# Performance work log

Measured on AMD Instinct MI355X. Metric: run time of the kernel, lower is better.

The kernel has to match this reference:

```python
import jax, jax.numpy as jnp
import numpy as np

B, T, F = 64, 512, 512      # batch, timesteps, raw feature dim
D_IN = 1024                 # input_layer units
H = 1024                    # hidden_units
D_OUT = 128                 # output_size


def setup_inputs() -> dict:
    key = jax.random.key(0)
    ks = jax.random.split(key, 10)
    def glorot(k, shape):
        lim = np.sqrt(6.0 / (shape[0] + shape[1])).astype(np.float32)
        return jax.random.uniform(k, shape, jnp.float32, -lim, lim)
    return {
        "x": jax.random.normal(ks[0], (B, T, F), jnp.float32),
        # input Dense (tanh)
        "Wi": glorot(ks[1], (F, D_IN)),
        "bi": jnp.zeros((D_IN,), jnp.float32),
        # LSTM layer 0: kernel, recurrent kernel, bias (init ones, gate order i,f,c,o)
        "W0": glorot(ks[2], (D_IN, 4 * H)),
        "U0": glorot(ks[3], (H, 4 * H)),
        "b0": jnp.ones((4 * H,), jnp.float32),
        # LSTM layer 1
        "W1": glorot(ks[4], (H, 4 * H)),
        "U1": glorot(ks[5], (H, 4 * H)),
        "b1": jnp.ones((4 * H,), jnp.float32),
        # output Dense (tanh)
        "Wo": glorot(ks[6], (H, D_OUT)),
        "bo": jnp.zeros((D_OUT,), jnp.float32),
    }


def _lstm_cell(x, h, c, W, U, b):
    # Keras LSTMCell gate order: i, f, c(candidate), o
    z = x @ W + h @ U + b                      # [B, 4H]
    zi, zf, zc, zo = jnp.split(z, 4, axis=-1)
    i = jax.nn.sigmoid(zi)
    f = jax.nn.sigmoid(zf)
    c_new = f * c + i * jnp.tanh(zc)
    h_new = jax.nn.sigmoid(zo) * jnp.tanh(c_new)
    return h_new, c_new


def reference(x, Wi, bi, W0, U0, b0, W1, U1, b1, Wo, bo):
    b = x.shape[0]
    h = W0.shape[1] // 4
    zeros = jnp.zeros((b, h), x.dtype)
    init = (zeros, zeros, zeros, zeros)  # h0, c0, h1, c1

    def step(carry, xt):
        h0, c0, h1, c1 = carry
        xin = jnp.tanh(xt @ Wi + bi)                    # input Dense
        h0, c0 = _lstm_cell(xin, h0, c0, W0, U0, b0)
        h1, c1 = _lstm_cell(h0, h1, c1, W1, U1, b1)
        return (h0, c0, h1, c1), None

    (h0, c0, h1, c1), _ = jax.lax.scan(step, init, jnp.swapaxes(x, 0, 1))
    return jnp.tanh(h1 @ Wo + bo)  # [B, D_OUT]
```

## Files before the change

kernel.cpp:

```cpp
#include <hip/hip_runtime.h>
#include <math.h>

#define BB 64
#define TT 512
#define FF 512
#define DIN 1024
#define HH 1024
#define G4 4096
#define DOUT 128

typedef _Float16 f16;
typedef _Float16 f16x4 __attribute__((ext_vector_type(4)));
typedef _Float16 f16x8 __attribute__((ext_vector_type(8)));
typedef float f32x4 __attribute__((ext_vector_type(4)));

__device__ __forceinline__ size_t afrag_off(int m, int k) {
    return (size_t)(((k >> 5) * 4 + (m >> 4)) * 512 + (((((k >> 3) & 3) << 4) | (m & 15)) * 8) + (k & 7));
}

__device__ __forceinline__ void store_b128_sc1(void* p, f32x4 v) {
    asm volatile("global_store_dwordx4 %0, %1, off sc1" :: "v"(p), "v"(v) : "memory");
}

__global__ __launch_bounds__(64) void k_pack(
    const float* __restrict__ W, const float* __restrict__ U, f16* __restrict__ out)
{
    const int kstep = blockIdx.x, cg = blockIdx.y, l = threadIdx.x;
    const int n = l & 15, q = l >> 4;
    const int stdcol = (n & 3) * HH + cg * 4 + (n >> 2);
    f16x8 v;
#pragma unroll
    for (int e = 0; e < 8; ++e) {
        int k = kstep * 32 + q * 8 + e;
        float s = (k < DIN) ? W[(size_t)k * G4 + stdcol] : U[(size_t)(k - DIN) * G4 + stdcol];
        v[e] = (f16)s;
    }
    *(f16x8*)(out + ((size_t)(cg * 64 + kstep) * 64 + l) * 8) = v;
}

__global__ __launch_bounds__(64) void k_pack_wi(
    const float* __restrict__ Wi, f16* __restrict__ out)
{
    const int kstep = blockIdx.x;
    const int nt    = blockIdx.y;
    const int l = threadIdx.x;
    const int n = nt * 16 + (l & 15), q = l >> 4;
    f16x8 v;
#pragma unroll
    for (int e = 0; e < 8; ++e)
        v[e] = (f16)Wi[(size_t)(kstep * 32 + q * 8 + e) * DIN + n];
    *(f16x8*)(out + ((size_t)(nt * 16 + kstep) * 64 + l) * 8) = v;
}

__global__ __launch_bounds__(256) void k_dense_in2(
    const float* __restrict__ x, const f16* __restrict__ pWi,
    const float* __restrict__ bi, f16* __restrict__ XinF)
{
    extern __shared__ f16 xs[];
    const int t = blockIdx.x;
    const int tid = threadIdx.x;

#pragma unroll
    for (int it = 0; it < 32; ++it) {
        int idx = tid + it * 256;
        int r = idx >> 7, c4 = idx & 127;
        float4 v = *(const float4*)(x + ((size_t)r * TT + t) * FF + c4 * 4);
        f16x4 hv = {(f16)v.x, (f16)v.y, (f16)v.z, (f16)v.w};
        *(f16x4*)(xs + (size_t)r * 520 + c4 * 4) = hv;
    }
    __syncthreads();

    const int w = tid >> 6, lane = tid & 63;
    const int col = lane & 15, rq = lane >> 4;
#pragma unroll 1
    for (int g = 0; g < 4; ++g) {
        f32x4 acc[4][4];
#pragma unroll
        for (int a = 0; a < 4; ++a)
#pragma unroll
            for (int b = 0; b < 4; ++b) acc[a][b] = (f32x4){0.f, 0.f, 0.f, 0.f};
#pragma unroll 2
        for (int ks2 = 0; ks2 < 16; ++ks2) {
            f16x8 bf[4];
#pragma unroll
            for (int nn = 0; nn < 4; ++nn)
                bf[nn] = *(const f16x8*)(pWi + ((size_t)((w * 16 + g * 4 + nn) * 16 + ks2) * 64 + lane) * 8);
#pragma unroll
            for (int mt = 0; mt < 4; ++mt) {
                f16x8 af = *(const f16x8*)(xs + (size_t)(mt * 16 + col) * 520 + ks2 * 32 + rq * 8);
#pragma unroll
                for (int nn = 0; nn < 4; ++nn)
                    acc[mt][nn] = __builtin_amdgcn_mfma_f32_16x16x32_f16(af, bf[nn], acc[mt][nn], 0, 0, 0);
            }
        }
#pragma unroll
        for (int nn = 0; nn < 4; ++nn) {
            const int j = (w * 16 + g * 4 + nn) * 16 + col;
            const float bb = bi[j];
#pragma unroll
            for (int mt = 0; mt < 4; ++mt)
#pragma unroll
                for (int r = 0; r < 4; ++r)
                    XinF[(size_t)t * (BB * DIN) + afrag_off(mt * 16 + rq * 4 + r, j)]
                        = (f16)tanhf(acc[mt][nn][r] + bb);
        }
    }
}

__global__ __launch_bounds__(512, 2) void k_persist(
    const f16* __restrict__ XinF,
    f16* __restrict__ h0b_, f16* __restrict__ h1b_,
    const f16* __restrict__ pW0, const f16* __restrict__ pW1,
    const float* __restrict__ b0, const float* __restrict__ b1,
    unsigned* __restrict__ flags)
{
    extern __shared__ char smem[];
    f16*   bsh = (f16*)smem;
    float* red = (float*)(smem + 131072);

    const int lay = blockIdx.x & 1;
    const int cgb = blockIdx.x >> 1;
    const int tid = threadIdx.x;
    const int wv = tid >> 6, lane = tid & 63;
    const int kq = wv >> 1, mh = wv & 1;

    unsigned* fl   = flags + (lay ? 1024 : 0);
    unsigned* goO  = flags + 2048 + (lay ? 32 : 0);
    unsigned* go0p = flags + 2048;
    const bool isAgg = (cgb == 0);

    {
        const f16x8* s8 = (const f16x8*)((lay ? pW1 : pW0) + (size_t)(cgb * 2) * 64 * 512);
        f16x8* d8 = (f16x8*)bsh;
#pragma unroll
        for (int it = 0; it < 16; ++it) d8[tid + it * 512] = s8[tid + it * 512];
    }

    const float* bias = lay ? b1 : b0;
    const int erow = tid & 63, ejl = (tid >> 6) & 3;
    const int emt = erow >> 4, esub = erow & 15;
    const int eslq = (esub >> 2) << 4, ereg = esub & 3;
    float bz[2][4];
    float creg[2] = {0.f, 0.f};
    if (tid < 256) {
#pragma unroll
        for (int n = 0; n < 2; ++n) {
            const int jg = (cgb * 2 + n) * 4 + ejl;
#pragma unroll
            for (int g = 0; g < 4; ++g) bz[n][g] = bias[g * HH + jg];
        }
    }

    const size_t HBUF = (size_t)BB * DIN;
    const f16* bq = bsh + (size_t)(kq * 16 * 64 + lane) * 8;
    __syncthreads();

    for (int p = 0; p <= TT; ++p) {
        if (lay == 0 && p == TT) break;
        const bool active = lay ? (p >= 1) : true;

        if (active) {
            const f16* Abase;
            if (lay == 0) Abase = (kq < 2) ? (XinF + (size_t)p * HBUF) : (h0b_ + (size_t)p * HBUF);
            else          Abase = (kq < 2) ? (h0b_ + (size_t)p * HBUF) : (h1b_ + (size_t)(p - 1) * HBUF);
            f16* hw = lay ? (h1b_ + (size_t)p * HBUF) : (h0b_ + (size_t)(p + 1) * HBUF);
            const f16* Ap = Abase + (size_t)(((kq & 1) * 64 + mh * 2) * 512) + (size_t)lane * 8;

            f16x8 a0v[16], a1v[16];
            const bool pre = (lay == 0) && (kq < 2);
            if (pre) {
#pragma unroll
                for (int ii = 0; ii < 16; ++ii) {
                    a0v[ii] = *(const f16x8*)(Ap + (size_t)(ii * 4) * 512);
                    a1v[ii] = *(const f16x8*)(Ap + (size_t)(ii * 4 + 1) * 512);
                }
            }

            if (lay == 0) {
                if (p > 0) {
                    if (tid == 0)
                        while (__hip_atomic_load(go0p, __ATOMIC_RELAXED, __HIP_MEMORY_SCOPE_AGENT) < (unsigned)p)
                            __builtin_amdgcn_s_sleep(1);
                    __syncthreads();
                }
            } else {
                if (tid == 0) {
                    while (__hip_atomic_load(go0p, __ATOMIC_RELAXED, __HIP_MEMORY_SCOPE_AGENT) < (unsigned)p)
                        __builtin_amdgcn_s_sleep(1);
                    while (__hip_atomic_load(goO, __ATOMIC_RELAXED, __HIP_MEMORY_SCOPE_AGENT) < (unsigned)p)
                        __builtin_amdgcn_s_sleep(1);
                }
                __syncthreads();
            }

            if (!pre) {
#pragma unroll
                for (int ii = 0; ii < 16; ++ii) {
                    a0v[ii] = *(const f16x8*)(Ap + (size_t)(ii * 4) * 512);
                    a1v[ii] = *(const f16x8*)(Ap + (size_t)(ii * 4 + 1) * 512);
                }
            }

            f32x4 acc00 = {0.f,0.f,0.f,0.f}, acc01 = {0.f,0.f,0.f,0.f};
            f32x4 acc10 = {0.f,0.f,0.f,0.f}, acc11 = {0.f,0.f,0.f,0.f};
#pragma unroll
            for (int ii = 0; ii < 16; ++ii) {
                f16x8 bb0 = *(const f16x8*)(bq + (size_t)ii * 512);
                f16x8 bb1 = *(const f16x8*)(bq + 32768 + (size_t)ii * 512);
                acc00 = __builtin_amdgcn_mfma_f32_16x16x32_f16(a0v[ii], bb0, acc00, 0, 0, 0);
                acc01 = __builtin_amdgcn_mfma_f32_16x16x32_f16(a0v[ii], bb1, acc01, 0, 0, 0);
                acc10 = __builtin_amdgcn_mfma_f32_16x16x32_f16(a1v[ii], bb0, acc10, 0, 0, 0);
                acc11 = __builtin_amdgcn_mfma_f32_16x16x32_f16(a1v[ii], bb1, acc11, 0, 0, 0);
            }

            f16 hvv[2];
#pragma unroll
            for (int n = 0; n < 2; ++n) {
                f32x4 t0 = n ? acc01 : acc00;
                f32x4 t1 = n ? acc11 : acc10;
                *(f32x4*)(red + (size_t)(kq * 4 + mh * 2)     * 260 + lane * 4) = t0;
                *(f32x4*)(red + (size_t)(kq * 4 + mh * 2 + 1) * 260 + lane * 4) = t1;
                __syncthreads();
                if (tid < 256) {
                    float z[4];
#pragma unroll
                    for (int g = 0; g < 4; ++g) {
                        const int sl = eslq | (ejl * 4 + g);
                        float s = 0.f;
#pragma unroll
                        for (int k2 = 0; k2 < 4; ++k2)
                            s += red[(size_t)(k2 * 4 + emt) * 260 + sl * 4 + ereg];
                        z[g] = s + bz[n][g];
                    }
                    const float ig = 1.f / (1.f + expf(-z[0]));
                    const float fg = 1.f / (1.f + expf(-z[1]));
                    const float cc = tanhf(z[2]);
                    const float og = 1.f / (1.f + expf(-z[3]));
                    const float cn = fg * creg[n] + ig * cc;
                    creg[n] = cn;
                    hvv[n] = (f16)(og * tanhf(cn));
                }
                __syncthreads();
            }

            f16* hrow = (f16*)red;
            if (tid < 256) {
                hrow[erow * 8 + ejl]     = hvv[0];
                hrow[erow * 8 + 4 + ejl] = hvv[1];
            }
            __syncthreads();
            if (tid < 64) {
                f32x4 v = *(f32x4*)(hrow + tid * 8);
                store_b128_sc1(hw + afrag_off(tid, cgb * 8), v);
            }
        }

        asm volatile("s_waitcnt vmcnt(0)" ::: "memory");
        __syncthreads();
        const unsigned tgt = (unsigned)(p + 1);
        if (tid == 0)
            __hip_atomic_store(&fl[cgb], tgt, __ATOMIC_RELAXED, __HIP_MEMORY_SCOPE_AGENT);
        if (isAgg) {
            if (tid < 64) {
                for (;;) {
                    bool ok = (__hip_atomic_load(&fl[lane], __ATOMIC_RELAXED, __HIP_MEMORY_SCOPE_AGENT) >= tgt)
                           && (__hip_atomic_load(&fl[lane + 64], __ATOMIC_RELAXED, __HIP_MEMORY_SCOPE_AGENT) >= tgt);
                    if (__all(ok)) break;
                    __builtin_amdgcn_s_sleep(1);
                }
                if (tid == 0)
                    __hip_atomic_store(goO, tgt, __ATOMIC_RELAXED, __HIP_MEMORY_SCOPE_AGENT);
            }
        }
    }
}

__global__ __launch_bounds__(128) void k_out(
    const f16* __restrict__ h1f, const float* __restrict__ Wo,
    const float* __restrict__ bo, float* __restrict__ out)
{
    __shared__ float hs[HH];
    const int b = blockIdx.x;
    for (int i = threadIdx.x; i < HH; i += 128) hs[i] = (float)h1f[afrag_off(b, i)];
    __syncthreads();
    const int o = threadIdx.x;
    float acc = 0.f;
    for (int k = 0; k < HH; ++k) acc += hs[k] * Wo[k * DOUT + o];
    out[b * DOUT + o] = tanhf(acc + bo[o]);
}

extern "C" void kernel_launch(void* const* d_in, const int* in_sizes, int n_in,
                              void* d_out, int out_size, void* d_ws, size_t ws_size,
                              hipStream_t stream)
{
    const float* x  = (const float*)d_in[0];
    const float* Wi = (const float*)d_in[1];
    const float* bi = (const float*)d_in[2];
    const float* W0 = (const float*)d_in[3];
    const float* U0 = (const float*)d_in[4];
    const float* b0 = (const float*)d_in[5];
    const float* W1 = (const float*)d_in[6];
    const float* U1 = (const float*)d_in[7];
    const float* b1 = (const float*)d_in[8];
    const float* Wo = (const float*)d_in[9];
    const float* bo = (const float*)d_in[10];
    float* out = (float*)d_out;

    f16* ws16 = (f16*)d_ws;
    const size_t HBUF = (size_t)BB * DIN;
    f16* XinF = ws16;
    f16* pW0  = XinF + (size_t)TT * HBUF;
    f16* pW1  = pW0 + (size_t)2048 * G4;
    f16* pWi  = pW1 + (size_t)2048 * G4;
    f16* h0   = pWi + (size_t)FF * DIN;
    f16* h1   = h0 + (size_t)513 * HBUF;
    unsigned* flags = (unsigned*)(h1 + (size_t)513 * HBUF);

    hipMemsetAsync(h0, 0, HBUF * sizeof(f16), stream);
    hipMemsetAsync(h1, 0, HBUF * sizeof(f16), stream);
    hipMemsetAsync(flags, 0, 16384, stream);

    k_pack<<<dim3(64, 256), 64, 0, stream>>>(W0, U0, pW0);
    k_pack<<<dim3(64, 256), 64, 0, stream>>>(W1, U1, pW1);
    k_pack_wi<<<dim3(16, 64), 64, 0, stream>>>(Wi, pWi);

    hipFuncSetAttribute((const void*)k_dense_in2,
                        hipFuncAttributeMaxDynamicSharedMemorySize, 66560);
    k_dense_in2<<<TT, 256, 66560, stream>>>(x, pWi, bi, XinF);

    {
        const int smem_bytes = 131072 + 16640;
        hipFuncSetAttribute((const void*)k_persist,
                            hipFuncAttributeMaxDynamicSharedMemorySize, smem_bytes);
        const f16* XinF_c = XinF;
        const f16* pW0_c = pW0;
        const f16* pW1_c = pW1;
        f16 *h0_v = h0, *h1_v = h1;
        const float *b0_v = b0, *b1_v = b1;
        unsigned* flags_v = flags;
        void* kargs[] = {
            (void*)&XinF_c,
            (void*)&h0_v, (void*)&h1_v,
            (void*)&pW0_c, (void*)&pW1_c,
            (void*)&b0_v, (void*)&b1_v,
            (void*)&flags_v
        };
        hipLaunchCooperativeKernel((void*)k_persist, dim3(256), dim3(512),
                                   kargs, smem_bytes, stream);
    }

    k_out<<<BB, 128, 0, stream>>>(h1 + (size_t)512 * HBUF, Wo, bo, out);
}
```

Before: 3.376 ms.

## Replace aggregator barrier with direct flag polling and keep weights in registers

Removes the per-layer aggregator block that collected all 128 per-block flags and then published a go counter. Consumers now poll all 128 producer flags directly, cutting one global hop per timestep from the critical path. Recurrent weight fragments are now held in VGPRs rather than LDS. The gate reduction is rebuilt around a padded row-major LDS buffer that needs a single barrier instead of one per column group. Holding 256 f16x8 operand registers under launch_bounds(512,2) raises register pressure and risks spills, and every block now polls all flags at once, which adds contention.

```diff
diff --git a/kernel.cpp b/kernel.cpp
--- a/kernel.cpp
+++ b/kernel.cpp
@@ -22,6 +22,35 @@
     asm volatile("global_store_dwordx4 %0, %1, off sc1" :: "v"(p), "v"(v) : "memory");
 }
 
+__device__ __forceinline__ void poll128(const unsigned* base, int lane, unsigned tgt) {
+    for (;;) {
+        bool ok = (__hip_atomic_load(&base[lane], __ATOMIC_RELAXED, __HIP_MEMORY_SCOPE_AGENT) >= tgt)
+               && (__hip_atomic_load(&base[lane + 64], __ATOMIC_RELAXED, __HIP_MEMORY_SCOPE_AGENT) >= tgt);
+        if (__all(ok)) return;
+        __builtin_amdgcn_s_sleep(1);
+    }
+}
+
+__device__ __forceinline__ void gemm_half(
+    const f16* __restrict__ Ap,
+    const f16x8 (&bb0)[16], const f16x8 (&bb1)[16],
+    f32x4& acc00, f32x4& acc01, f32x4& acc10, f32x4& acc11)
+{
+    f16x8 a0v[16], a1v[16];
+#pragma unroll
+    for (int ii = 0; ii < 16; ++ii) {
+        a0v[ii] = *(const f16x8*)(Ap + (size_t)(ii * 4) * 512);
+        a1v[ii] = *(const f16x8*)(Ap + (size_t)(ii * 4 + 1) * 512);
+    }
+#pragma unroll
+    for (int ii = 0; ii < 16; ++ii) {
+        acc00 = __builtin_amdgcn_mfma_f32_16x16x32_f16(a0v[ii], bb0[ii], acc00, 0, 0, 0);
+        acc01 = __builtin_amdgcn_mfma_f32_16x16x32_f16(a0v[ii], bb1[ii], acc01, 0, 0, 0);
+        acc10 = __builtin_amdgcn_mfma_f32_16x16x32_f16(a1v[ii], bb0[ii], acc10, 0, 0, 0);
+        acc11 = __builtin_amdgcn_mfma_f32_16x16x32_f16(a1v[ii], bb1[ii], acc11, 0, 0, 0);
+    }
+}
+
 __global__ __launch_bounds__(64) void k_pack(
     const float* __restrict__ W, const float* __restrict__ U, f16* __restrict__ out)
 {
@@ -115,8 +144,8 @@
     unsigned* __restrict__ flags)
 {
     extern __shared__ char smem[];
-    f16*   bsh = (f16*)smem;
-    float* red = (float*)(smem + 131072);
+    float* buf  = (float*)smem;
+    f16*   hrow = (f16*)(smem + 40960);
 
     const int lay = blockIdx.x & 1;
     const int cgb = blockIdx.x >> 1;
@@ -124,22 +153,23 @@
     const int wv = tid >> 6, lane = tid & 63;
     const int kq = wv >> 1, mh = wv & 1;
 
-    unsigned* fl   = flags + (lay ? 1024 : 0);
-    unsigned* goO  = flags + 2048 + (lay ? 32 : 0);
-    unsigned* go0p = flags + 2048;
-    const bool isAgg = (cgb == 0);
-
+    unsigned* fl0 = flags;
+    unsigned* fl1 = flags + 1024;
+    unsigned* flOwn = lay ? fl1 : fl0;
+
+    f16x8 bb0[16], bb1[16];
     {
-        const f16x8* s8 = (const f16x8*)((lay ? pW1 : pW0) + (size_t)(cgb * 2) * 64 * 512);
-        f16x8* d8 = (f16x8*)bsh;
-#pragma unroll
-        for (int it = 0; it < 16; ++it) d8[tid + it * 512] = s8[tid + it * 512];
+        const f16* gB = (lay ? pW1 : pW0)
+                      + ((size_t)(cgb * 2) * 64 + (size_t)kq * 16) * 512 + (size_t)lane * 8;
+#pragma unroll
+        for (int ii = 0; ii < 16; ++ii) {
+            bb0[ii] = *(const f16x8*)(gB + (size_t)ii * 512);
+            bb1[ii] = *(const f16x8*)(gB + 32768 + (size_t)ii * 512);
+        }
     }
 
     const float* bias = lay ? b1 : b0;
     const int erow = tid & 63, ejl = (tid >> 6) & 3;
-    const int emt = erow >> 4, esub = erow & 15;
-    const int eslq = (esub >> 2) << 4, ereg = esub & 3;
     float bz[2][4];
     float creg[2] = {0.f, 0.f};
     if (tid < 256) {
@@ -152,8 +182,7 @@
     }
 
     const size_t HBUF = (size_t)BB * DIN;
-    const f16* bq = bsh + (size_t)(kq * 16 * 64 + lane) * 8;
-    __syncthreads();
+    const int colw = lane & 15, rg = lane >> 4;
 
     for (int p = 0; p <= TT; ++p) {
         if (lay == 0 && p == TT) break;
@@ -166,89 +195,64 @@
             f16* hw = lay ? (h1b_ + (size_t)p * HBUF) : (h0b_ + (size_t)(p + 1) * HBUF);
             const f16* Ap = Abase + (size_t)(((kq & 1) * 64 + mh * 2) * 512) + (size_t)lane * 8;
 
-            f16x8 a0v[16], a1v[16];
+            f32x4 acc00 = {0.f,0.f,0.f,0.f}, acc01 = {0.f,0.f,0.f,0.f};
+            f32x4 acc10 = {0.f,0.f,0.f,0.f}, acc11 = {0.f,0.f,0.f,0.f};
+
             const bool pre = (lay == 0) && (kq < 2);
-            if (pre) {
-#pragma unroll
-                for (int ii = 0; ii < 16; ++ii) {
-                    a0v[ii] = *(const f16x8*)(Ap + (size_t)(ii * 4) * 512);
-                    a1v[ii] = *(const f16x8*)(Ap + (size_t)(ii * 4 + 1) * 512);
-                }
-            }
+            if (pre) gemm_half(Ap, bb0, bb1, acc00, acc01, acc10, acc11);
 
             if (lay == 0) {
                 if (p > 0) {
-                    if (tid == 0)
-                        while (__hip_atomic_load(go0p, __ATOMIC_RELAXED, __HIP_MEMORY_SCOPE_AGENT) < (unsigned)p)
-                            __builtin_amdgcn_s_sleep(1);
+                    if (tid < 64) poll128(fl0, lane, (unsigned)p);
                     __syncthreads();
                 }
             } else {
-                if (tid == 0) {
-                    while (__hip_atomic_load(go0p, __ATOMIC_RELAXED, __HIP_MEMORY_SCOPE_AGENT) < (unsigned)p)
-                        __builtin_amdgcn_s_sleep(1);
-                    while (__hip_atomic_load(goO, __ATOMIC_RELAXED, __HIP_MEMORY_SCOPE_AGENT) < (unsigned)p)
-                        __builtin_amdgcn_s_sleep(1);
+                if (tid < 128) poll128((tid < 64) ? fl0 : fl1, lane, (unsigned)p);
+                __syncthreads();
+            }
+
+            if (!pre) gemm_half(Ap, bb0, bb1, acc00, acc01, acc10, acc11);
+
+            {
+                float* t00 = buf + (size_t)(kq * 2 + 0) * 1280 + ((mh * 2) * 16 + rg * 4) * 20 + colw;
+                float* t01 = buf + (size_t)(kq * 2 + 1) * 1280 + ((mh * 2) * 16 + rg * 4) * 20 + colw;
+                float* t10 = t00 + 16 * 20;
+                float* t11 = t01 + 16 * 20;
+#pragma unroll
+                for (int r = 0; r < 4; ++r) {
+                    t00[r * 20] = acc00[r];
+                    t01[r * 20] = acc01[r];
+                    t10[r * 20] = acc10[r];
+                    t11[r * 20] = acc11[r];
                 }
-                __syncthreads();
-            }
-
-            if (!pre) {
-#pragma unroll
-                for (int ii = 0; ii < 16; ++ii) {
-                    a0v[ii] = *(const f16x8*)(Ap + (size_t)(ii * 4) * 512);
-                    a1v[ii] = *(const f16x8*)(Ap + (size_t)(ii * 4 + 1) * 512);
-                }
-            }
-
-            f32x4 acc00 = {0.f,0.f,0.f,0.f}, acc01 = {0.f,0.f,0.f,0.f};
-            f32x4 acc10 = {0.f,0.f,0.f,0.f}, acc11 = {0.f,0.f,0.f,0.f};
-#pragma unroll
-            for (int ii = 0; ii < 16; ++ii) {
-                f16x8 bb0 = *(const f16x8*)(bq + (size_t)ii * 512);
-                f16x8 bb1 = *(const f16x8*)(bq + 32768 + (size_t)ii * 512);
-                acc00 = __builtin_amdgcn_mfma_f32_16x16x32_f16(a0v[ii], bb0, acc00, 0, 0, 0);
-                acc01 = __builtin_amdgcn_mfma_f32_16x16x32_f16(a0v[ii], bb1, acc01, 0, 0, 0);
-                acc10 = __builtin_amdgcn_mfma_f32_16x16x32_f16(a1v[ii], bb0, acc10, 0, 0, 0);
-                acc11 = __builtin_amdgcn_mfma_f32_16x16x32_f16(a1v[ii], bb1, acc11, 0, 0, 0);
-            }
-
-            f16 hvv[2];
-#pragma unroll
-            for (int n = 0; n < 2; ++n) {
-                f32x4 t0 = n ? acc01 : acc00;
-                f32x4 t1 = n ? acc11 : acc10;
-                *(f32x4*)(red + (size_t)(kq * 4 + mh * 2)     * 260 + lane * 4) = t0;
-                *(f32x4*)(red + (size_t)(kq * 4 + mh * 2 + 1) * 260 + lane * 4) = t1;
-                __syncthreads();
-                if (tid < 256) {
-                    float z[4];
-#pragma unroll
-                    for (int g = 0; g < 4; ++g) {
-                        const int sl = eslq | (ejl * 4 + g);
-                        float s = 0.f;
-#pragma unroll
-                        for (int k2 = 0; k2 < 4; ++k2)
-                            s += red[(size_t)(k2 * 4 + emt) * 260 + sl * 4 + ereg];
-                        z[g] = s + bz[n][g];
-                    }
-                    const float ig = 1.f / (1.f + expf(-z[0]));
-                    const float fg = 1.f / (1.f + expf(-z[1]));
-                    const float cc = tanhf(z[2]);
-                    const float og = 1.f / (1.f + expf(-z[3]));
+            }
+            __syncthreads();
+
+            if (tid < 256) {
+                f16 hvv[2];
+#pragma unroll
+                for (int n = 0; n < 2; ++n) {
+                    f32x4 z = {0.f,0.f,0.f,0.f};
+#pragma unroll
+                    for (int k2 = 0; k2 < 4; ++k2)
+                        z += *(const f32x4*)(buf + (size_t)(k2 * 2 + n) * 1280 + erow * 20 + ejl * 4);
+                    const float z0 = z[0] + bz[n][0];
+                    const float z1 = z[1] + bz[n][1];
+                    const float z2 = z[2] + bz[n][2];
+                    const float z3 = z[3] + bz[n][3];
+                    const float ig = 1.f / (1.f + expf(-z0));
+                    const float fg = 1.f / (1.f + expf(-z1));
+                    const float cc = tanhf(z2);
+                    const float og = 1.f / (1.f + expf(-z3));
                     const float cn = fg * creg[n] + ig * cc;
                     creg[n] = cn;
                     hvv[n] = (f16)(og * tanhf(cn));
                 }
-                __syncthreads();
-            }
-
-            f16* hrow = (f16*)red;
-            if (tid < 256) {
                 hrow[erow * 8 + ejl]     = hvv[0];
                 hrow[erow * 8 + 4 + ejl] = hvv[1];
             }
             __syncthreads();
+
             if (tid < 64) {
                 f32x4 v = *(f32x4*)(hrow + tid * 8);
                 store_b128_sc1(hw + afrag_off(tid, cgb * 8), v);
@@ -256,22 +260,9 @@
         }
 
         asm volatile("s_waitcnt vmcnt(0)" ::: "memory");
-        __syncthreads();
-        const unsigned tgt = (unsigned)(p + 1);
         if (tid == 0)
-            __hip_atomic_store(&fl[cgb], tgt, __ATOMIC_RELAXED, __HIP_MEMORY_SCOPE_AGENT);
-        if (isAgg) {
-            if (tid < 64) {
-                for (;;) {
-                    bool ok = (__hip_atomic_load(&fl[lane], __ATOMIC_RELAXED, __HIP_MEMORY_SCOPE_AGENT) >= tgt)
-                           && (__hip_atomic_load(&fl[lane + 64], __ATOMIC_RELAXED, __HIP_MEMORY_SCOPE_AGENT) >= tgt);
-                    if (__all(ok)) break;
-                    __builtin_amdgcn_s_sleep(1);
-                }
-                if (tid == 0)
-                    __hip_atomic_store(goO, tgt, __ATOMIC_RELAXED, __HIP_MEMORY_SCOPE_AGENT);
-            }
-        }
+            __hip_atomic_store(&flOwn[cgb], (unsigned)(p + 1),
+                               __ATOMIC_RELAXED, __HIP_MEMORY_SCOPE_AGENT);
     }
 }
 
@@ -329,7 +320,7 @@
     k_dense_in2<<<TT, 256, 66560, stream>>>(x, pWi, bi, XinF);
 
     {
-        const int smem_bytes = 131072 + 16640;
+        const int smem_bytes = 98304;
         hipFuncSetAttribute((const void*)k_persist,
                             hipFuncAttributeMaxDynamicSharedMemorySize, smem_bytes);
         const f16* XinF_c = XinF;
```

New measurement: 5.212 ms. 54.4% more time.
